# Optimization experiments

Measured on AMD Instinct MI355X. Metric: run time of the kernel, lower is better.

## Reference

```python
import jax, jax.numpy as jnp
import numpy as np

NUM_BLOCKS = 32
BLOCK_CAP = 1024
KEY_DIM = 256
VALUE_DIM = 256
HIDDEN = 768
INIT_SCALE = 0.02
LN_EPS = 1e-5


def setup_inputs() -> dict:
    key = jax.random.key(0)
    ks = jax.random.split(key, 8)
    B, S = 4, 2048
    hidden_states = jax.random.normal(ks[0], (B, S, HIDDEN), dtype=jnp.float32)
    # variable per-block fill levels (>=1 so every block participates)
    block_usage = jax.random.randint(ks[1], (NUM_BLOCKS,), 1, BLOCK_CAP + 1, dtype=jnp.int32)
    # learned params
    Wk = jax.random.normal(ks[2], (HIDDEN, KEY_DIM), dtype=jnp.float32) * 0.02
    bk = jnp.zeros((KEY_DIM,), dtype=jnp.float32)
    ln_w = jnp.ones((KEY_DIM,), dtype=jnp.float32)
    ln_b = jnp.zeros((KEY_DIM,), dtype=jnp.float32)
    memory_keys = jax.random.normal(ks[3], (NUM_BLOCKS, BLOCK_CAP, KEY_DIM), dtype=jnp.float32) * INIT_SCALE
    memory_values = jax.random.normal(ks[4], (NUM_BLOCKS, BLOCK_CAP, VALUE_DIM), dtype=jnp.float32) * INIT_SCALE
    Wo = jax.random.normal(ks[5], (VALUE_DIM, HIDDEN), dtype=jnp.float32) * 0.02
    bo = jnp.zeros((HIDDEN,), dtype=jnp.float32)
    return {
        "hidden_states": hidden_states,
        "Wk": Wk, "bk": bk,
        "ln_w": ln_w, "ln_b": ln_b,
        "memory_keys": memory_keys, "memory_values": memory_values,
        "Wo": Wo, "bo": bo,
        "block_usage": block_usage,
    }


def reference(hidden_states, Wk, bk, ln_w, ln_b, memory_keys, memory_values, Wo, bo, block_usage):
    B, S, H = hidden_states.shape
    # query projection + layernorm (query_norm)
    q = hidden_states @ Wk + bk                      # [B,S,Dk]
    mu = q.mean(-1, keepdims=True)
    var = ((q - mu) ** 2).mean(-1, keepdims=True)
    q = (q - mu) * jax.lax.rsqrt(var + LN_EPS) * ln_w + ln_b
    q = q.reshape(B * S, KEY_DIM)                    # [N,Dk]
    # per-block attention over valid (used) prefix, summed over blocks
    scores = jnp.einsum('nd,bcd->nbc', q, memory_keys) / np.sqrt(KEY_DIM)  # [N,Blk,Cap]
    valid = jnp.arange(BLOCK_CAP)[None, :] < block_usage[:, None]          # [Blk,Cap]
    scores = jnp.where(valid[None], scores, -jnp.inf)
    attn = jax.nn.softmax(scores, axis=-1)           # softmax within each block's prefix
    retrieved = jnp.einsum('nbc,bcd->nd', attn, memory_values)  # sum over blocks
    out = retrieved @ Wo + bo
    return out.reshape(B, S, H)
```

## Files before the change

### kernel.cpp

```cpp
#include <hip/hip_runtime.h>
#include <hip/hip_bf16.h>

#define NBLK 32
#define CAP  1024
#define DK   256
#define DV   256
#define HID  768
#define NQ   8192

#define NEG_INF (-__builtin_inff())

typedef __bf16 bfv8 __attribute__((ext_vector_type(8)));
typedef float  f32x4  __attribute__((ext_vector_type(4)));
typedef float  f32x16 __attribute__((ext_vector_type(16)));

__device__ __forceinline__ unsigned short f2bf(float x){
  unsigned int u = __float_as_uint(x);
  u += 0x7FFFu + ((u >> 16) & 1u);
  return (unsigned short)(u >> 16);
}

#define GLOAD16(gp, lp) __builtin_amdgcn_global_load_lds( \
    (const __attribute__((address_space(1))) unsigned int*)(gp), \
    (__attribute__((address_space(3))) unsigned int*)(lp), 16, 0, 0)

__global__ void k_cast(const float* __restrict__ src, unsigned short* __restrict__ dst, int n){
  int i = (blockIdx.x * blockDim.x + threadIdx.x) * 4;
  if (i >= n) return;
  float4 v = *reinterpret_cast<const float4*>(src + i);
  union { unsigned short s[4]; uint2 u; } o;
  o.s[0] = f2bf(v.x); o.s[1] = f2bf(v.y); o.s[2] = f2bf(v.z); o.s[3] = f2bf(v.w);
  *reinterpret_cast<uint2*>(dst + i) = o.u;
}

__global__ void k_transpose_cast(const float* __restrict__ src, unsigned short* __restrict__ dst,
                                 int R, int C){
  __shared__ float tile[64][65];
  int r0 = blockIdx.x * 64, c0 = blockIdx.y * 64;
  size_t base = (size_t)blockIdx.z * (size_t)R * (size_t)C;
  int t = threadIdx.x;
  #pragma unroll
  for (int it = 0; it < 16; ++it){
    int idx = it * 256 + t;
    int ri = idx >> 6, ci = idx & 63;
    tile[ri][ci] = src[base + (size_t)(r0 + ri) * C + (c0 + ci)];
  }
  __syncthreads();
  #pragma unroll
  for (int it = 0; it < 16; ++it){
    int idx = it * 256 + t;
    int ci = idx >> 6, ri = idx & 63;
    dst[base + (size_t)(c0 + ci) * R + (r0 + ri)] = f2bf(tile[ri][ci]);
  }
}

__global__ __launch_bounds__(64)
void k_qproj2(const float* __restrict__ hs, const unsigned short* __restrict__ WkT,
              const float* __restrict__ bk, const float* __restrict__ lnw,
              const float* __restrict__ lnb, unsigned short* __restrict__ qb){
  int l = threadIdx.x, fr = l & 15, g = l >> 4;
  int r0 = blockIdx.x * 16;
  f32x4 acc[16];
  #pragma unroll
  for (int i = 0; i < 16; ++i) acc[i] = f32x4{0.f,0.f,0.f,0.f};
  for (int k0 = 0; k0 < HID; k0 += 32){
    const float* ap = hs + (size_t)(r0 + fr) * HID + k0 + g * 8;
    float4 a0 = *reinterpret_cast<const float4*>(ap);
    float4 a1 = *reinterpret_cast<const float4*>(ap + 4);
    union { unsigned short u[8]; bfv8 v; } A;
    A.u[0]=f2bf(a0.x); A.u[1]=f2bf(a0.y); A.u[2]=f2bf(a0.z); A.u[3]=f2bf(a0.w);
    A.u[4]=f2bf(a1.x); A.u[5]=f2bf(a1.y); A.u[6]=f2bf(a1.z); A.u[7]=f2bf(a1.w);
    #pragma unroll
    for (int dt = 0; dt < 16; ++dt){
      bfv8 b = *reinterpret_cast<const bfv8*>(WkT + (size_t)(dt*16 + fr) * HID + k0 + g*8);
      acc[dt] = __builtin_amdgcn_mfma_f32_16x16x32_bf16(A.v, b, acc[dt], 0, 0, 0);
    }
  }
  float sum[4] = {0,0,0,0}, sq[4] = {0,0,0,0};
  #pragma unroll
  for (int dt = 0; dt < 16; ++dt){
    float bkv = bk[dt*16 + fr];
    #pragma unroll
    for (int r = 0; r < 4; ++r){
      float v = acc[dt][r] + bkv;
      acc[dt][r] = v;
      sum[r] += v; sq[r] += v * v;
    }
  }
  #pragma unroll
  for (int r = 0; r < 4; ++r){
    float s = sum[r], q = sq[r];
    s += __shfl_xor(s, 1);  q += __shfl_xor(q, 1);
    s += __shfl_xor(s, 2);  q += __shfl_xor(q, 2);
    s += __shfl_xor(s, 4);  q += __shfl_xor(q, 4);
    s += __shfl_xor(s, 8);  q += __shfl_xor(q, 8);
    sum[r] = s; sq[r] = q;
  }
  #pragma unroll
  for (int dt = 0; dt < 16; ++dt){
    float w = lnw[dt*16 + fr], bb = lnb[dt*16 + fr];
    #pragma unroll
    for (int r = 0; r < 4; ++r){
      float mu  = sum[r] * (1.f/256.f);
      float var = sq[r] * (1.f/256.f) - mu * mu;
      float rsq = rsqrtf(var + 1e-5f);
      float v   = ((acc[dt][r] - mu) * rsq * w + bb) * 0.0625f;
      qb[(size_t)(r0 + 4*g + r) * DK + dt*16 + fr] = f2bf(v);
    }
  }
}

template<int FOLD>
__global__ __launch_bounds__(256, 2)
void k_attn3(const unsigned short* __restrict__ qb, const unsigned short* __restrict__ Kb,
             const unsigned short* __restrict__ VTb, const int* __restrict__ usage,
             float* __restrict__ dst){
  __shared__ unsigned short Ksm[2][32*256];
  __shared__ unsigned short Vsm[2][128*64];
  __shared__ unsigned short Pt[4][32*40];
  const int t = threadIdx.x, w = t >> 6, l = t & 63;
  const int lq = l & 31, hi = l >> 5;
  const int qtile = blockIdx.x, bg = blockIdx.y;
  const int qrow = qtile * 128 + w * 32 + lq;

  bfv8 qf[16];
  #pragma unroll
  for (int ks = 0; ks < 16; ++ks)
    qf[ks] = *reinterpret_cast<const bfv8*>(qb + (size_t)qrow * DK + ks*16 + hi*8);

  int krow[4], koff[4], voff[4];
  #pragma unroll
  for (int i = 0; i < 4; ++i){
    int idx = w*4 + i;
    int row = idx*2 + hi;
    krow[i] = row;
    koff[i] = ((l & 31) ^ (row & 7)) * 8;
    int prow = idx*8 + (l >> 3);
    int n = (l & 7) ^ (prow & 7);
    int dv = 2*prow + (n >> 2);
    voff[i] = dv * CAP + (n & 3) * 8;
  }
  int bs[4], us[4], nts[4];
  #pragma unroll
  for (int i = 0; i < 4; ++i){ bs[i] = bg + i*8; us[i] = usage[bs[i]]; nts[i] = (us[i] + 31) >> 5; }

  unsigned short* Pw = &Pt[w][0];

  auto STAGE = [&](int buf, int b, int tt){
    const unsigned short* Kbase = Kb  + (size_t)b * CAP * DK;
    const unsigned short* Vbase = VTb + (size_t)b * DV * CAP;
    int c0 = tt * 32;
    #pragma unroll
    for (int i = 0; i < 4; ++i){
      GLOAD16(Kbase + (size_t)(c0 + krow[i]) * DK + koff[i], &Ksm[buf][(w*4 + i) * 512]);
      GLOAD16(Vbase + voff[i] + c0,                          &Vsm[buf][(w*4 + i) * 512]);
    }
  };

  int cur = 0;
  STAGE(0, bs[0], 0);
  __syncthreads();

  #pragma unroll 1
  for (int i = 0; i < 4; ++i){
    const int u = us[i], nt = nts[i];
    float m = NEG_INF, lsum = 0.f;
    f32x16 O[8];
    #pragma unroll
    for (int r = 0; r < 8; ++r)
      #pragma unroll
      for (int j = 0; j < 16; ++j) O[r][j] = 0.f;

    #pragma unroll 1
    for (int tt = 0; tt < nt; ++tt){
      bool isLast = (i == 3) && (tt == nt - 1);
      if (!isLast){
        int ni  = (tt + 1 < nt) ? i : i + 1;
        int ntt = (tt + 1 < nt) ? tt + 1 : 0;
        STAGE(cur ^ 1, bs[ni & 3], ntt);
      }
      int c0 = tt * 32;
      f32x16 s;
      #pragma unroll
      for (int j = 0; j < 16; ++j) s[j] = 0.f;
      const unsigned short* Kc = &Ksm[cur][0];
      #pragma unroll
      for (int ks = 0; ks < 16; ++ks){
        bfv8 kf = *reinterpret_cast<const bfv8*>(Kc + lq*DK + (((2*ks + hi) ^ (lq & 7)) * 8));
        s = __builtin_amdgcn_mfma_f32_32x32x16_bf16(kf, qf[ks], s, 0, 0, 0);
      }
      float tm = NEG_INF;
      #pragma unroll
      for (int r = 0; r < 16; ++r){
        int kv = (r & 3) + 8*(r >> 2) + 4*hi;
        if (c0 + kv >= u) s[r] = NEG_INF;
        tm = fmaxf(tm, s[r]);
      }
      tm = fmaxf(tm, __shfl_xor(tm, 32));
      float mn = fmaxf(m, tm);
      if (!__all(tm - m <= 8.f)){
        float sc = __expf(m - mn);
        m = mn; lsum *= sc;
        #pragma unroll
        for (int r = 0; r < 8; ++r) O[r] *= sc;
      }
      float rs = 0.f;
      #pragma unroll
      for (int r = 0; r < 16; ++r){
        float e = __expf(s[r] - m);
        s[r] = e; rs += e;
      }
      rs += __shfl_xor(rs, 32);
      lsum += rs;
      #pragma unroll
      for (int blk = 0; blk < 4; ++blk){
        unsigned int w0 = (unsigned int)f2bf(s[4*blk])   | ((unsigned int)f2bf(s[4*blk+1]) << 16);
        unsigned int w1 = (unsigned int)f2bf(s[4*blk+2]) | ((unsigned int)f2bf(s[4*blk+3]) << 16);
        *reinterpret_cast<uint2*>(Pw + lq*40 + blk*8 + hi*4) = uint2{w0, w1};
      }
      asm volatile("s_waitcnt lgkmcnt(0)" ::: "memory");
      __builtin_amdgcn_sched_barrier(0);
      bfv8 pa0 = *reinterpret_cast<const bfv8*>(Pw + lq*40 + hi*8);
      bfv8 pa1 = *reinterpret_cast<const bfv8*>(Pw + lq*40 + 16 + hi*8);
      const unsigned short* Vc = &Vsm[cur][0];
      #pragma unroll
      for (int rt = 0; rt < 8; ++rt){
        int dv = rt*32 + lq;
        int prow = dv >> 1;
        int a4 = (dv & 1) * 4;
        int n0 = (a4 + hi)     ^ (prow & 7);
        int n1 = (a4 + 2 + hi) ^ (prow & 7);
        bfv8 v0 = *reinterpret_cast<const bfv8*>(Vc + prow*64 + n0*8);
        bfv8 v1 = *reinterpret_cast<const bfv8*>(Vc + prow*64 + n1*8);
        O[rt] = __builtin_amdgcn_mfma_f32_32x32x16_bf16(v0, pa0, O[rt], 0, 0, 0);
        O[rt] = __builtin_amdgcn_mfma_f32_32x32x16_bf16(v1, pa1, O[rt], 0, 0, 0);
      }
      __syncthreads();
      cur ^= 1;
    }
    float inv = 1.f / lsum;
    if constexpr (FOLD == 0){
      float* pb = dst + ((size_t)bg * NQ + qrow) * DV;
      #pragma unroll
      for (int rt = 0; rt < 8; ++rt){
        #pragma unroll
        for (int blk = 0; blk < 4; ++blk){
          int dv0 = rt*32 + blk*8 + hi*4;
          float4* p4 = reinterpret_cast<float4*>(pb + dv0);
          float4 vv;
          vv.x = O[rt][blk*4 + 0] * inv;
          vv.y = O[rt][blk*4 + 1] * inv;
          vv.z = O[rt][blk*4 + 2] * inv;
          vv.w = O[rt][blk*4 + 3] * inv;
          if (i > 0){
            float4 o = *p4;
            vv.x += o.x; vv.y += o.y; vv.z += o.z; vv.w += o.w;
          }
          *p4 = vv;
        }
      }
    } else {
      float* pb = dst + (size_t)qrow * DV;
      #pragma unroll
      for (int rt = 0; rt < 8; ++rt){
        #pragma unroll
        for (int blk = 0; blk < 4; ++blk){
          int dv0 = rt*32 + blk*8 + hi*4;
          #pragma unroll
          for (int j = 0; j < 4; ++j)
            atomicAdd(pb + dv0 + j, O[rt][blk*4 + j] * inv);
        }
      }
    }
  }
}

__global__ void k_reduce(const float* __restrict__ partial, float* __restrict__ retr){
  int i = (blockIdx.x * 256 + threadIdx.x) * 4;
  float4 acc = {0.f, 0.f, 0.f, 0.f};
  #pragma unroll
  for (int bg = 0; bg < 8; ++bg){
    float4 v = *reinterpret_cast<const float4*>(partial + (size_t)bg * NQ * DV + i);
    acc.x += v.x; acc.y += v.y; acc.z += v.z; acc.w += v.w;
  }
  *reinterpret_cast<float4*>(retr + i) = acc;
}

__global__ __launch_bounds__(64)
void k_outproj3(const float* __restrict__ retr, const unsigned short* __restrict__ WoT,
                const float* __restrict__ bo, float* __restrict__ out){
  int l = threadIdx.x, fr = l & 15, g = l >> 4;
  int r0 = blockIdx.x * 16, c0 = blockIdx.y * 256;
  f32x4 acc[16];
  #pragma unroll
  for (int i = 0; i < 16; ++i) acc[i] = f32x4{0.f,0.f,0.f,0.f};
  #pragma unroll
  for (int k0 = 0; k0 < DV; k0 += 32){
    const float* ap = retr + (size_t)(r0 + fr) * DV + k0 + g*8;
    float4 a0 = *reinterpret_cast<const float4*>(ap);
    float4 a1 = *reinterpret_cast<const float4*>(ap + 4);
    union { unsigned short u[8]; bfv8 v; } A;
    A.u[0]=f2bf(a0.x); A.u[1]=f2bf(a0.y); A.u[2]=f2bf(a0.z); A.u[3]=f2bf(a0.w);
    A.u[4]=f2bf(a1.x); A.u[5]=f2bf(a1.y); A.u[6]=f2bf(a1.z); A.u[7]=f2bf(a1.w);
    #pragma unroll
    for (int dt = 0; dt < 16; ++dt){
      bfv8 b = *reinterpret_cast<const bfv8*>(WoT + (size_t)(c0 + dt*16 + fr) * DV + k0 + g*8);
      acc[dt] = __builtin_amdgcn_mfma_f32_16x16x32_bf16(A.v, b, acc[dt], 0, 0, 0);
    }
  }
  #pragma unroll
  for (int dt = 0; dt < 16; ++dt){
    float bv = bo[c0 + dt*16 + fr];
    #pragma unroll
    for (int r = 0; r < 4; ++r)
      out[(size_t)(r0 + 4*g + r) * HID + c0 + dt*16 + fr] = acc[dt][r] + bv;
  }
}

extern "C" void kernel_launch(void* const* d_in, const int* in_sizes, int n_in,
                              void* d_out, int out_size, void* d_ws, size_t ws_size,
                              hipStream_t stream){
  const float* hs  = (const float*)d_in[0];
  const float* Wk  = (const float*)d_in[1];
  const float* bk  = (const float*)d_in[2];
  const float* lnw = (const float*)d_in[3];
  const float* lnb = (const float*)d_in[4];
  const float* MK  = (const float*)d_in[5];
  const float* MV  = (const float*)d_in[6];
  const float* Wo  = (const float*)d_in[7];
  const float* bo  = (const float*)d_in[8];
  const int*   bu  = (const int*)d_in[9];
  float* out = (float*)d_out;

  char* ws = (char*)d_ws;
  unsigned short* qb   = (unsigned short*)(ws);
  unsigned short* Kb   = (unsigned short*)(ws + (size_t)( 4u<<20));
  unsigned short* VTb  = (unsigned short*)(ws + (size_t)(20u<<20));
  unsigned short* WkT  = (unsigned short*)(ws + (size_t)(36u<<20));
  unsigned short* WoT  = (unsigned short*)(ws + (size_t)(36u<<20) + 393216);
  float*          retr = (float*)(ws + (size_t)(37u<<20));
  float*        partial = (float*)(ws + (size_t)(45u<<20));

  const bool big_ws = ws_size >= ((size_t)110 << 20);

  k_cast<<<dim3(8192), dim3(256), 0, stream>>>(MK, Kb, NBLK * CAP * DK);
  k_transpose_cast<<<dim3(16, 4, 32), dim3(256), 0, stream>>>(MV, VTb, CAP, DV);
  k_transpose_cast<<<dim3(12, 4, 1),  dim3(256), 0, stream>>>(Wk, WkT, HID, DK);
  k_transpose_cast<<<dim3(4, 12, 1),  dim3(256), 0, stream>>>(Wo, WoT, DV, HID);
  k_qproj2<<<dim3(512), dim3(64), 0, stream>>>(hs, WkT, bk, lnw, lnb, qb);

  if (big_ws){
    k_attn3<0><<<dim3(64, 8), dim3(256), 0, stream>>>(qb, Kb, VTb, bu, partial);
    k_reduce<<<dim3(2048), dim3(256), 0, stream>>>(partial, retr);
  } else {
    hipMemsetAsync(retr, 0, (size_t)NQ * DV * sizeof(float), stream);
    k_attn3<1><<<dim3(64, 8), dim3(256), 0, stream>>>(qb, Kb, VTb, bu, retr);
  }
  k_outproj3<<<dim3(512, 3), dim3(64), 0, stream>>>(retr, WoT, bo, out);
}
```

Measured before the change: 613.1 us.

## Pre-pack K/V/Q into MFMA fragment order and load directly from global

Memory keys and values are now repacked into the exact per-lane MFMA fragment layout, so the attention kernel loads operands straight from global/L2 with coalesced 16-byte reads. This removes the LDS double-buffered staging and the per-tile __syncthreads. The query projection writes q in fragment order as well. The grid is reordered so block groups vary fastest, which should improve L2 sharing of K/V across workgroups. Two independent MFMA accumulator chains shorten the dependency chain, setprio is raised around the PV loop, and the partial-buffer path with its reduce kernel is dropped in favour of always using atomics. The risks are global-load latency now sitting directly in the MFMA loop without LDS reuse across the 4 waves, and heavier atomic traffic.

```diff
diff --git a/kernel.cpp b/kernel.cpp
--- a/kernel.cpp
+++ b/kernel.cpp
@@ -20,19 +20,6 @@
   return (unsigned short)(u >> 16);
 }
 
-#define GLOAD16(gp, lp) __builtin_amdgcn_global_load_lds( \
-    (const __attribute__((address_space(1))) unsigned int*)(gp), \
-    (__attribute__((address_space(3))) unsigned int*)(lp), 16, 0, 0)
-
-__global__ void k_cast(const float* __restrict__ src, unsigned short* __restrict__ dst, int n){
-  int i = (blockIdx.x * blockDim.x + threadIdx.x) * 4;
-  if (i >= n) return;
-  float4 v = *reinterpret_cast<const float4*>(src + i);
-  union { unsigned short s[4]; uint2 u; } o;
-  o.s[0] = f2bf(v.x); o.s[1] = f2bf(v.y); o.s[2] = f2bf(v.z); o.s[3] = f2bf(v.w);
-  *reinterpret_cast<uint2*>(dst + i) = o.u;
-}
-
 __global__ void k_transpose_cast(const float* __restrict__ src, unsigned short* __restrict__ dst,
                                  int R, int C){
   __shared__ float tile[64][65];
@@ -54,10 +41,36 @@
   }
 }
 
+__global__ void k_packK(const float* __restrict__ MK, unsigned short* __restrict__ Kp){
+  int id = blockIdx.x * 256 + threadIdx.x;
+  int l  = id & 63, ks = (id >> 6) & 15, tt = (id >> 10) & 31, b = id >> 15;
+  int lq = l & 31, hi = l >> 5;
+  const float* sp = MK + ((size_t)(b * CAP + tt * 32 + lq)) * DK + ks * 16 + hi * 8;
+  float4 a0 = *reinterpret_cast<const float4*>(sp);
+  float4 a1 = *reinterpret_cast<const float4*>(sp + 4);
+  union { unsigned short s[8]; int4 v; } o;
+  o.s[0]=f2bf(a0.x); o.s[1]=f2bf(a0.y); o.s[2]=f2bf(a0.z); o.s[3]=f2bf(a0.w);
+  o.s[4]=f2bf(a1.x); o.s[5]=f2bf(a1.y); o.s[6]=f2bf(a1.z); o.s[7]=f2bf(a1.w);
+  *reinterpret_cast<int4*>(Kp + (size_t)id * 8) = o.v;
+}
+
+__global__ void k_packV(const float* __restrict__ MV, unsigned short* __restrict__ Vp){
+  int id = blockIdx.x * 256 + threadIdx.x;
+  int l  = id & 63, ks2 = (id >> 6) & 1, rt = (id >> 7) & 7, tt = (id >> 10) & 31, b = id >> 15;
+  int lq = l & 31, hi = l >> 5;
+  int c0 = tt * 32 + ks2 * 16 + hi * 8;
+  int dv = rt * 32 + lq;
+  union { unsigned short s[8]; int4 v; } o;
+  #pragma unroll
+  for (int j = 0; j < 8; ++j)
+    o.s[j] = f2bf(MV[((size_t)(b * CAP + c0 + j)) * DV + dv]);
+  *reinterpret_cast<int4*>(Vp + (size_t)id * 8) = o.v;
+}
+
 __global__ __launch_bounds__(64)
-void k_qproj2(const float* __restrict__ hs, const unsigned short* __restrict__ WkT,
+void k_qproj3(const float* __restrict__ hs, const unsigned short* __restrict__ WkT,
               const float* __restrict__ bk, const float* __restrict__ lnw,
-              const float* __restrict__ lnb, unsigned short* __restrict__ qb){
+              const float* __restrict__ lnb, unsigned short* __restrict__ qp){
   int l = threadIdx.x, fr = l & 15, g = l >> 4;
   int r0 = blockIdx.x * 16;
   f32x4 acc[16];
@@ -105,65 +118,38 @@
       float var = sq[r] * (1.f/256.f) - mu * mu;
       float rsq = rsqrtf(var + 1e-5f);
       float v   = ((acc[dt][r] - mu) * rsq * w + bb) * 0.0625f;
-      qb[(size_t)(r0 + 4*g + r) * DK + dt*16 + fr] = f2bf(v);
-    }
-  }
-}
-
-template<int FOLD>
+      int qrow = r0 + 4*g + r;
+      int d    = dt*16 + fr;
+      int g0q = qrow >> 5, lqq = qrow & 31;
+      int ksq = d >> 4, hiq = (d >> 3) & 1, jq = d & 7;
+      qp[(((size_t)g0q*16 + ksq)*64 + hiq*32 + lqq)*8 + jq] = f2bf(v);
+    }
+  }
+}
+
 __global__ __launch_bounds__(256, 2)
-void k_attn3(const unsigned short* __restrict__ qb, const unsigned short* __restrict__ Kb,
-             const unsigned short* __restrict__ VTb, const int* __restrict__ usage,
-             float* __restrict__ dst){
-  __shared__ unsigned short Ksm[2][32*256];
-  __shared__ unsigned short Vsm[2][128*64];
-  __shared__ unsigned short Pt[4][32*40];
+void k_attn4(const unsigned short* __restrict__ qp, const unsigned short* __restrict__ Kp,
+             const unsigned short* __restrict__ Vp, const int* __restrict__ usage,
+             float* __restrict__ retr){
+  __shared__ unsigned short Pt[4][32*44];
   const int t = threadIdx.x, w = t >> 6, l = t & 63;
   const int lq = l & 31, hi = l >> 5;
-  const int qtile = blockIdx.x, bg = blockIdx.y;
-  const int qrow = qtile * 128 + w * 32 + lq;
+  const int bg = blockIdx.x, qt = blockIdx.y;
+  const int g0 = qt * 4 + w;
+  const int qrow = g0 * 32 + lq;
 
   bfv8 qf[16];
   #pragma unroll
   for (int ks = 0; ks < 16; ++ks)
-    qf[ks] = *reinterpret_cast<const bfv8*>(qb + (size_t)qrow * DK + ks*16 + hi*8);
-
-  int krow[4], koff[4], voff[4];
-  #pragma unroll
-  for (int i = 0; i < 4; ++i){
-    int idx = w*4 + i;
-    int row = idx*2 + hi;
-    krow[i] = row;
-    koff[i] = ((l & 31) ^ (row & 7)) * 8;
-    int prow = idx*8 + (l >> 3);
-    int n = (l & 7) ^ (prow & 7);
-    int dv = 2*prow + (n >> 2);
-    voff[i] = dv * CAP + (n & 3) * 8;
-  }
-  int bs[4], us[4], nts[4];
-  #pragma unroll
-  for (int i = 0; i < 4; ++i){ bs[i] = bg + i*8; us[i] = usage[bs[i]]; nts[i] = (us[i] + 31) >> 5; }
+    qf[ks] = *reinterpret_cast<const bfv8*>(qp + ((size_t)g0*16 + ks)*512 + l*8);
 
   unsigned short* Pw = &Pt[w][0];
-
-  auto STAGE = [&](int buf, int b, int tt){
-    const unsigned short* Kbase = Kb  + (size_t)b * CAP * DK;
-    const unsigned short* Vbase = VTb + (size_t)b * DV * CAP;
-    int c0 = tt * 32;
-    #pragma unroll
-    for (int i = 0; i < 4; ++i){
-      GLOAD16(Kbase + (size_t)(c0 + krow[i]) * DK + koff[i], &Ksm[buf][(w*4 + i) * 512]);
-      GLOAD16(Vbase + voff[i] + c0,                          &Vsm[buf][(w*4 + i) * 512]);
-    }
-  };
-
-  int cur = 0;
-  STAGE(0, bs[0], 0);
-  __syncthreads();
 
   #pragma unroll 1
   for (int i = 0; i < 4; ++i){
-    const int u = us[i], nt = nts[i];
+    const int b = bg + i * 8;
+    const int u = usage[b];
+    const int nt = (u + 31) >> 5;
     float m = NEG_INF, lsum = 0.f;
     f32x16 O[8];
     #pragma unroll
@@ -173,22 +159,21 @@
 
     #pragma unroll 1
     for (int tt = 0; tt < nt; ++tt){
-      bool isLast = (i == 3) && (tt == nt - 1);
-      if (!isLast){
-        int ni  = (tt + 1 < nt) ? i : i + 1;
-        int ntt = (tt + 1 < nt) ? tt + 1 : 0;
-        STAGE(cur ^ 1, bs[ni & 3], ntt);
-      }
-      int c0 = tt * 32;
+      const int c0 = tt * 32;
+      const unsigned short* Kt = Kp + ((size_t)(b*32 + tt) * 16) * 512;
+      f32x16 s0, s1;
+      #pragma unroll
+      for (int j = 0; j < 16; ++j){ s0[j] = 0.f; s1[j] = 0.f; }
+      #pragma unroll
+      for (int ks = 0; ks < 8; ++ks){
+        bfv8 k0 = *reinterpret_cast<const bfv8*>(Kt + (size_t)(2*ks)*512 + l*8);
+        bfv8 k1 = *reinterpret_cast<const bfv8*>(Kt + (size_t)(2*ks+1)*512 + l*8);
+        s0 = __builtin_amdgcn_mfma_f32_32x32x16_bf16(k0, qf[2*ks],   s0, 0, 0, 0);
+        s1 = __builtin_amdgcn_mfma_f32_32x32x16_bf16(k1, qf[2*ks+1], s1, 0, 0, 0);
+      }
       f32x16 s;
       #pragma unroll
-      for (int j = 0; j < 16; ++j) s[j] = 0.f;
-      const unsigned short* Kc = &Ksm[cur][0];
-      #pragma unroll
-      for (int ks = 0; ks < 16; ++ks){
-        bfv8 kf = *reinterpret_cast<const bfv8*>(Kc + lq*DK + (((2*ks + hi) ^ (lq & 7)) * 8));
-        s = __builtin_amdgcn_mfma_f32_32x32x16_bf16(kf, qf[ks], s, 0, 0, 0);
-      }
+      for (int j = 0; j < 16; ++j) s[j] = s0[j] + s1[j];
       float tm = NEG_INF;
       #pragma unroll
       for (int r = 0; r < 16; ++r){
@@ -216,74 +201,36 @@
       for (int blk = 0; blk < 4; ++blk){
         unsigned int w0 = (unsigned int)f2bf(s[4*blk])   | ((unsigned int)f2bf(s[4*blk+1]) << 16);
         unsigned int w1 = (unsigned int)f2bf(s[4*blk+2]) | ((unsigned int)f2bf(s[4*blk+3]) << 16);
-        *reinterpret_cast<uint2*>(Pw + lq*40 + blk*8 + hi*4) = uint2{w0, w1};
+        *reinterpret_cast<uint2*>(Pw + lq*44 + blk*8 + hi*4) = uint2{w0, w1};
       }
       asm volatile("s_waitcnt lgkmcnt(0)" ::: "memory");
       __builtin_amdgcn_sched_barrier(0);
-      bfv8 pa0 = *reinterpret_cast<const bfv8*>(Pw + lq*40 + hi*8);
-      bfv8 pa1 = *reinterpret_cast<const bfv8*>(Pw + lq*40 + 16 + hi*8);
-      const unsigned short* Vc = &Vsm[cur][0];
+      bfv8 pa0 = *reinterpret_cast<const bfv8*>(Pw + lq*44 + hi*8);
+      bfv8 pa1 = *reinterpret_cast<const bfv8*>(Pw + lq*44 + 16 + hi*8);
+      const unsigned short* Vt = Vp + ((size_t)(b*32 + tt) * 16) * 512;
+      __builtin_amdgcn_s_setprio(1);
       #pragma unroll
       for (int rt = 0; rt < 8; ++rt){
-        int dv = rt*32 + lq;
-        int prow = dv >> 1;
-        int a4 = (dv & 1) * 4;
-        int n0 = (a4 + hi)     ^ (prow & 7);
-        int n1 = (a4 + 2 + hi) ^ (prow & 7);
-        bfv8 v0 = *reinterpret_cast<const bfv8*>(Vc + prow*64 + n0*8);
-        bfv8 v1 = *reinterpret_cast<const bfv8*>(Vc + prow*64 + n1*8);
+        bfv8 v0 = *reinterpret_cast<const bfv8*>(Vt + (size_t)(rt*2+0)*512 + l*8);
+        bfv8 v1 = *reinterpret_cast<const bfv8*>(Vt + (size_t)(rt*2+1)*512 + l*8);
         O[rt] = __builtin_amdgcn_mfma_f32_32x32x16_bf16(v0, pa0, O[rt], 0, 0, 0);
         O[rt] = __builtin_amdgcn_mfma_f32_32x32x16_bf16(v1, pa1, O[rt], 0, 0, 0);
       }
-      __syncthreads();
-      cur ^= 1;
+      __builtin_amdgcn_s_setprio(0);
     }
     float inv = 1.f / lsum;
-    if constexpr (FOLD == 0){
-      float* pb = dst + ((size_t)bg * NQ + qrow) * DV;
-      #pragma unroll
-      for (int rt = 0; rt < 8; ++rt){
+    float* pb = retr + (size_t)qrow * DV;
+    #pragma unroll
+    for (int rt = 0; rt < 8; ++rt){
+      #pragma unroll
+      for (int blk = 0; blk < 4; ++blk){
+        int dv0 = rt*32 + blk*8 + hi*4;
         #pragma unroll
-        for (int blk = 0; blk < 4; ++blk){
-          int dv0 = rt*32 + blk*8 + hi*4;
-          float4* p4 = reinterpret_cast<float4*>(pb + dv0);
-          float4 vv;
-          vv.x = O[rt][blk*4 + 0] * inv;
-          vv.y = O[rt][blk*4 + 1] * inv;
-          vv.z = O[rt][blk*4 + 2] * inv;
-          vv.w = O[rt][blk*4 + 3] * inv;
-          if (i > 0){
-            float4 o = *p4;
-            vv.x += o.x; vv.y += o.y; vv.z += o.z; vv.w += o.w;
-          }
-          *p4 = vv;
-        }
-      }
-    } else {
-      float* pb = dst + (size_t)qrow * DV;
-      #pragma unroll
-      for (int rt = 0; rt < 8; ++rt){
-        #pragma unroll
-        for (int blk = 0; blk < 4; ++blk){
-          int dv0 = rt*32 + blk*8 + hi*4;
-          #pragma unroll
-          for (int j = 0; j < 4; ++j)
-            atomicAdd(pb + dv0 + j, O[rt][blk*4 + j] * inv);
-        }
-      }
-    }
-  }
-}
-
-__global__ void k_reduce(const float* __restrict__ partial, float* __restrict__ retr){
-  int i = (blockIdx.x * 256 + threadIdx.x) * 4;
-  float4 acc = {0.f, 0.f, 0.f, 0.f};
-  #pragma unroll
-  for (int bg = 0; bg < 8; ++bg){
-    float4 v = *reinterpret_cast<const float4*>(partial + (size_t)bg * NQ * DV + i);
-    acc.x += v.x; acc.y += v.y; acc.z += v.z; acc.w += v.w;
-  }
-  *reinterpret_cast<float4*>(retr + i) = acc;
+        for (int j = 0; j < 4; ++j)
+          atomicAdd(pb + dv0 + j, O[rt][blk*4 + j] * inv);
+      }
+    }
+  }
 }
 
 __global__ __launch_bounds__(64)
@@ -333,28 +280,18 @@
   float* out = (float*)d_out;
 
   char* ws = (char*)d_ws;
-  unsigned short* qb   = (unsigned short*)(ws);
-  unsigned short* Kb   = (unsigned short*)(ws + (size_t)( 4u<<20));
-  unsigned short* VTb  = (unsigned short*)(ws + (size_t)(20u<<20));
+  unsigned short* qp   = (unsigned short*)(ws);
+  unsigned short* Kp   = (unsigned short*)(ws + (size_t)( 4u<<20));
+  unsigned short* Vp   = (unsigned short*)(ws + (size_t)(20u<<20));
   unsigned short* WkT  = (unsigned short*)(ws + (size_t)(36u<<20));
   unsigned short* WoT  = (unsigned short*)(ws + (size_t)(36u<<20) + 393216);
   float*          retr = (float*)(ws + (size_t)(37u<<20));
-  float*        partial = (float*)(ws + (size_t)(45u<<20));
-
-  const bool big_ws = ws_size >= ((size_t)110 << 20);
-
-  k_cast<<<dim3(8192), dim3(256), 0, stream>>>(MK, Kb, NBLK * CAP * DK);
-  k_transpose_cast<<<dim3(16, 4, 32), dim3(256), 0, stream>>>(MV, VTb, CAP, DV);
-  k_transpose_cast<<<dim3(12, 4, 1),  dim3(256), 0, stream>>>(Wk, WkT, HID, DK);
-  k_transpose_cast<<<dim3(4, 12, 1),  dim3(256), 0, stream>>>(Wo, WoT, DV, HID);
-  k_qproj2<<<dim3(512), dim3(64), 0, stream>>>(hs, WkT, bk, lnw, lnb, qb);
-
-  if (big_ws){
-    k_attn3<0><<<dim3(64, 8), dim3(256), 0, stream>>>(qb, Kb, VTb, bu, partial);
-    k_reduce<<<dim3(2048), dim3(256), 0, stream>>>(partial, retr);
-  } else {
-    hipMemsetAsync(retr, 0, (size_t)NQ * DV * sizeof(float), stream);
-    k_attn3<1><<<dim3(64, 8), dim3(256), 0, stream>>>(qb, Kb, VTb, bu, retr);
-  }
+  k_packK<<<dim3(4096), dim3(256), 0, stream>>>(MK, Kp);
+  k_packV<<<dim3(4096), dim3(256), 0, stream>>>(MV, Vp);
+  k_transpose_cast<<<dim3(12, 4, 1), dim3(256), 0, stream>>>(Wk, WkT, HID, DK);
+  k_transpose_cast<<<dim3(4, 12, 1), dim3(256), 0, stream>>>(Wo, WoT, DV, HID);
+  k_qproj3<<<dim3(512), dim3(64), 0, stream>>>(hs, WkT, bk, lnw, lnb, qp);
+  hipMemsetAsync(retr, 0, (size_t)NQ * DV * sizeof(float), stream);
+  k_attn4<<<dim3(8, 64), dim3(256), 0, stream>>>(qp, Kp, Vp, bu, retr);
   k_outproj3<<<dim3(512, 3), dim3(64), 0, stream>>>(retr, WoT, bo, out);
 }
```

After: 1.859 ms. 3.03x slower.
